# Kernel tuning notes

Hardware: AMD Instinct MI355X
Metric: run time of the kernel (lower is better)

Reference implementation:

```python
import jax, jax.numpy as jnp
import numpy as np


def recursive_fht(x):
    # Faithful vectorized version of the module's recursive butterfly FHT
    # (twiddle = cas(2*pi*n/N), no flipped-odd term, exactly as in the source).
    N = x.shape[-1]
    if N == 1:
        return x
    e = recursive_fht(x[..., ::2])
    o = recursive_fht(x[..., 1::2])
    n = jnp.arange(N // 2, dtype=x.dtype)
    t = jnp.cos(2 * jnp.pi * n / N) + jnp.sin(2 * jnp.pi * n / N)
    return jnp.concatenate([e + t * o, e - t * o], axis=-1)


def compl_mul1d(x1, x2):
    # x1: [B, i, modes], x2: [i, o, modes]; flips along axis 0 as in the source
    x1f = x1[::-1]
    x2f = x2[::-1]
    return 0.5 * (jnp.einsum('bix,iox->box', x1, x2)
                  - jnp.einsum('bix,iox->box', x1f, x2f)
                  + jnp.einsum('bix,iox->box', x1, x2f)
                  + jnp.einsum('bix,iox->box', x1f, x2))


def idht(X):
    # Inverse discrete Hartley transform via the cas matrix (DHT is an
    # involution up to 1/K). K = N//2+1 is not a power of 2, so a dense
    # transform is used. Compute-bound batched GEMM.
    K = X.shape[-1]
    n = jnp.arange(K, dtype=X.dtype)
    ang = 2.0 * jnp.pi * jnp.outer(n, n) / K
    cas = jnp.cos(ang) + jnp.sin(ang)  # [K, K]
    return jnp.einsum('bck,kn->bcn', X, cas) / K


def setup_inputs() -> dict:
    key = jax.random.key(0)
    k1, k2 = jax.random.split(key)
    B, Cin, Cout, N, modes1 = 32, 64, 64, 4096, 1024
    x = jax.random.normal(k1, (B, Cin, N), dtype=jnp.float32)
    scale = 1.0 / (Cin * Cout)
    weights1 = scale * jax.random.uniform(k2, (Cin, Cout, modes1), dtype=jnp.float32)
    return {"x": x, "weights1": weights1, "modes1": modes1}


def reference(x, weights1, modes1):
    B, C, N = x.shape
    # dht with threshold=1.0: FHT along last axis, low-pass filter is a no-op
    x_ht = recursive_fht(x)
    K = N // 2 + 1
    out_ht = jnp.zeros((B, C, K), dtype=x.dtype)
    out_ht = out_ht.at[:, :, :modes1].set(compl_mul1d(x_ht[:, :, :modes1], weights1))
    return idht(out_ht)  # [B, C, N//2+1]
```

## Files before the change

kernel.cpp:

```cpp
#include <hip/hip_runtime.h>
#include <hip/hip_bf16.h>

#define BATCH 32
#define CIN   64
#define COUT  64
#define NFFT  4096
#define MODES 1024
#define KOUT  2049
#define NPAD  2112

typedef __bf16 bf16x8 __attribute__((ext_vector_type(8)));
typedef float  f32x4  __attribute__((ext_vector_type(4)));

#define AS1 __attribute__((address_space(1)))
#define AS3 __attribute__((address_space(3)))

static __device__ __forceinline__ void gl_lds16(const void* g, void* l) {
    __builtin_amdgcn_global_load_lds((const AS1 void*)g, (AS3 void*)l, 16, 0, 0);
}

static __device__ __forceinline__ float bf2f(unsigned short s) {
    return __uint_as_float(((unsigned)s) << 16);
}
static __device__ __forceinline__ void cvt8(bf16x8 v, f32x4& lo, f32x4& hi) {
    union { bf16x8 b; unsigned short s[8]; } u;
    u.b = v;
    lo = (f32x4){bf2f(u.s[0]), bf2f(u.s[1]), bf2f(u.s[2]), bf2f(u.s[3])};
    hi = (f32x4){bf2f(u.s[4]), bf2f(u.s[5]), bf2f(u.s[6]), bf2f(u.s[7])};
}
static __device__ __forceinline__ bf16x8 pack8(f32x4 lo, f32x4 hi) {
    union { bf16x8 b; unsigned short s[8]; } u;
    __hip_bfloat16 h;
    h = __float2bfloat16(lo.x); u.s[0] = *(unsigned short*)&h;
    h = __float2bfloat16(lo.y); u.s[1] = *(unsigned short*)&h;
    h = __float2bfloat16(lo.z); u.s[2] = *(unsigned short*)&h;
    h = __float2bfloat16(lo.w); u.s[3] = *(unsigned short*)&h;
    h = __float2bfloat16(hi.x); u.s[4] = *(unsigned short*)&h;
    h = __float2bfloat16(hi.y); u.s[5] = *(unsigned short*)&h;
    h = __float2bfloat16(hi.z); u.s[6] = *(unsigned short*)&h;
    h = __float2bfloat16(hi.w); u.s[7] = *(unsigned short*)&h;
    return u.b;
}

static __device__ __forceinline__ void bfly4(float eA, float eB, float oA, float oB,
                                             float t, float c0, float c1,
                                             float& w0, float& w1, float& w2, float& w3) {
    float PA = fmaf(t, oA, eA), MA = fmaf(-t, oA, eA);
    float PB = fmaf(t, oB, eB), MB = fmaf(-t, oB, eB);
    w0 = fmaf(c0, PB, PA);
    w2 = fmaf(-c0, PB, PA);
    w1 = fmaf(c1, MB, MA);
    w3 = fmaf(-c1, MB, MA);
}

#define NCHUNK ((NPAD / 16) * (MODES / 32) * 64)

__global__ void fill_tables(float* __restrict__ tw, __hip_bfloat16* __restrict__ c2f) {
    int gid = blockIdx.x * 256 + threadIdx.x;
    if (gid < NCHUNK) {
        int nl  = gid & 15;
        int kc  = (gid >> 4) & 3;
        int blk = gid >> 6;
        int kb  = blk & 31;
        int gn  = blk >> 5;
        int n = gn * 16 + nl;
        int kbase = kb * 32 + kc * 8;
        unsigned short v8[8];
        if (n < KOUT) {
#pragma unroll
            for (int j = 0; j < 8; ++j) {
                int k = kbase + j;
                int m = (k * n) % KOUT;
                float ang = 6.28318530717958647692f * (float)m / (float)KOUT;
                float v = (cosf(ang) + sinf(ang)) * (1.0f / (float)KOUT);
                __hip_bfloat16 h = __float2bfloat16(v);
                v8[j] = *(unsigned short*)&h;
            }
        } else {
#pragma unroll
            for (int j = 0; j < 8; ++j) v8[j] = 0;
        }
        *(ushort4*)((char*)c2f + (size_t)gid * 16)     = make_ushort4(v8[0], v8[1], v8[2], v8[3]);
        *(ushort4*)((char*)c2f + (size_t)gid * 16 + 8) = make_ushort4(v8[4], v8[5], v8[6], v8[7]);
    } else {
        int t = gid - NCHUNK;
        if (t < NFFT) {
            if (t == 0) { tw[0] = 1.0f; return; }
            int h = 1 << (31 - __clz(t));
            int n = t - h;
            float ang = 3.14159265358979323846f * (float)n / (float)h;
            tw[t] = cosf(ang) + sinf(ang);
        }
    }
}

__global__ __launch_bounds__(256) void fht_kernel(const float* __restrict__ x,
                                                  const float* __restrict__ tw,
                                                  __hip_bfloat16* __restrict__ xh) {
    __shared__ float ldsA[4352];
    __shared__ float ldsB[4352];
    const int t = threadIdx.x;
    const int row = blockIdx.x;
    const float* xr = x + (size_t)row * NFFT;

    float r[4][4];
#pragma unroll
    for (int a = 0; a < 4; ++a)
#pragma unroll
        for (int c = 0; c < 4; ++c)
            r[a][c] = xr[t + 256 * a + 1024 * c];

    float o1[4][4];
#pragma unroll
    for (int a = 0; a < 4; ++a) {
        float PA = r[a][0] + r[a][2], MA = r[a][0] - r[a][2];
        float PB = r[a][1] + r[a][3], MB = r[a][1] - r[a][3];
        o1[a][0] = PA + PB;
        o1[a][2] = PA - PB;
        o1[a][1] = MA + MB;
        o1[a][3] = MA - MB;
    }
    float o2[4][4];
#pragma unroll
    for (int kap = 0; kap < 4; ++kap) {
        float tt = tw[4 + kap], c0 = tw[8 + kap], c1 = tw[12 + kap];
        bfly4(o1[0][kap], o1[1][kap], o1[2][kap], o1[3][kap], tt, c0, c1,
              o2[kap][0], o2[kap][1], o2[kap][2], o2[kap][3]);
    }
#pragma unroll
    for (int kap = 0; kap < 4; ++kap)
#pragma unroll
        for (int c = 0; c < 4; ++c) {
            int p = t + 256 * kap + 1024 * c;
            ldsA[p + (p >> 4)] = o2[kap][c];
        }
    __syncthreads();

    const int kap2 = t >> 4, gp = t & 15;
    float r2[4][4];
#pragma unroll
    for (int a = 0; a < 4; ++a)
#pragma unroll
        for (int c = 0; c < 4; ++c) {
            int p = 256 * kap2 + gp + 16 * a + 64 * c;
            r2[a][c] = ldsA[p + (p >> 4)];
        }
    float o3[4][4];
    {
        float tt = tw[16 + kap2], c0 = tw[32 + kap2], c1 = tw[48 + kap2];
#pragma unroll
        for (int a = 0; a < 4; ++a)
            bfly4(r2[a][0], r2[a][1], r2[a][2], r2[a][3], tt, c0, c1,
                  o3[a][0], o3[a][1], o3[a][2], o3[a][3]);
    }
    float o4[4][4];
#pragma unroll
    for (int c = 0; c < 4; ++c) {
        int kap3 = kap2 + 16 * c;
        float tt = tw[64 + kap3], c0 = tw[128 + kap3], c1 = tw[192 + kap3];
        bfly4(o3[0][c], o3[1][c], o3[2][c], o3[3][c], tt, c0, c1,
              o4[c][0], o4[c][1], o4[c][2], o4[c][3]);
    }
#pragma unroll
    for (int c = 0; c < 4; ++c)
#pragma unroll
        for (int cc = 0; cc < 4; ++cc) {
            int p = t + 256 * c + 1024 * cc;
            ldsB[p + (p >> 4)] = o4[c][cc];
        }
    __syncthreads();

    float r3[4][4];
#pragma unroll
    for (int g = 0; g < 4; ++g)
#pragma unroll
        for (int c = 0; c < 4; ++c) {
            int p = 16 * t + g + 4 * c;
            r3[g][c] = ldsB[p + (p >> 4)];
        }
    float o5[4][4];
    {
        float tt = tw[256 + t], c0 = tw[512 + t], c1 = tw[768 + t];
#pragma unroll
        for (int g = 0; g < 4; ++g)
            bfly4(r3[g][0], r3[g][1], r3[g][2], r3[g][3], tt, c0, c1,
                  o5[g][0], o5[g][1], o5[g][2], o5[g][3]);
    }
    __hip_bfloat16* xo = xh + (size_t)row * MODES;
#pragma unroll
    for (int c = 0; c < 4; ++c) {
        float tt = tw[1024 + t + 256 * c];
        float c0 = tw[2048 + t + 256 * c];
        float PA = fmaf(tt, o5[2][c], o5[0][c]);
        float PB = fmaf(tt, o5[3][c], o5[1][c]);
        xo[t + 256 * c] = __float2bfloat16(fmaf(c0, PB, PA));
    }
}

__global__ __launch_bounds__(512) void mix_kernel(const __hip_bfloat16* __restrict__ xh,
                                                  const float* __restrict__ w,
                                                  __hip_bfloat16* __restrict__ y) {
    const int tid = threadIdx.x;
    const int kl  = tid & 1;
    const int og  = (tid >> 1) & 31;
    const int bpl = tid >> 6;
    const int bp  = blockIdx.y * 8 + bpl;
    const int rb  = (BATCH - 1) - bp;
    const int o   = blockIdx.z * 32 + og;
    const int k8  = blockIdx.x * 2 + kl;

    f32x4 accb0 = {0,0,0,0}, accb1 = {0,0,0,0};
    f32x4 accr0 = {0,0,0,0}, accr1 = {0,0,0,0};

    const __hip_bfloat16* xb  = xh + (size_t)(bp * CIN) * MODES + k8 * 8;
    const __hip_bfloat16* xrb = xh + (size_t)(rb * CIN) * MODES + k8 * 8;
    const float* wo = w + (size_t)o * MODES + k8 * 8;

#pragma unroll 4
    for (int i = 0; i < 32; ++i) {
        const int mi = 63 - i;
        bf16x8 xai = *(const bf16x8*)(xb  + (size_t)i  * MODES);
        bf16x8 xam = *(const bf16x8*)(xb  + (size_t)mi * MODES);
        bf16x8 xbi = *(const bf16x8*)(xrb + (size_t)i  * MODES);
        bf16x8 xbm = *(const bf16x8*)(xrb + (size_t)mi * MODES);
        f32x4 w1a = *(const f32x4*)(wo + (size_t)(i  * COUT) * MODES);
        f32x4 w1b = *(const f32x4*)(wo + (size_t)(i  * COUT) * MODES + 4);
        f32x4 w2a = *(const f32x4*)(wo + (size_t)(mi * COUT) * MODES);
        f32x4 w2b = *(const f32x4*)(wo + (size_t)(mi * COUT) * MODES + 4);

        f32x4 ai_lo, ai_hi, am_lo, am_hi, bi_lo, bi_hi, bm_lo, bm_hi;
        cvt8(xai, ai_lo, ai_hi);
        cvt8(xam, am_lo, am_hi);
        cvt8(xbi, bi_lo, bi_hi);
        cvt8(xbm, bm_lo, bm_hi);

        f32x4 sa0 = ai_lo + am_lo, sa1 = ai_hi + am_hi;
        f32x4 da0 = ai_lo - am_lo, da1 = ai_hi - am_hi;
        f32x4 sb0 = bi_lo + bm_lo, sb1 = bi_hi + bm_hi;
        f32x4 db0 = bi_lo - bm_lo, db1 = bi_hi - bm_hi;
        f32x4 wp0 = w1a + w2a, wm0 = w1a - w2a;
        f32x4 wp1 = w1b + w2b, wm1 = w1b - w2b;

        accb0 += sa0 * wp0 + db0 * wm0;
        accb1 += sa1 * wp1 + db1 * wm1;
        accr0 += sb0 * wp0 + da0 * wm0;
        accr1 += sb1 * wp1 + da1 * wm1;
    }

    bf16x8 vb = pack8(accb0 * 0.5f, accb1 * 0.5f);
    bf16x8 vr = pack8(accr0 * 0.5f, accr1 * 0.5f);
    *(bf16x8*)(y + (size_t)(bp * COUT + o) * MODES + k8 * 8) = vb;
    *(bf16x8*)(y + (size_t)(rb * COUT + o) * MODES + k8 * 8) = vr;
}

__global__ __launch_bounds__(128) void idht_mfma(const __hip_bfloat16* __restrict__ yh,
                                                 const __hip_bfloat16* __restrict__ c2f,
                                                 float* __restrict__ out) {
    __shared__ __align__(16) char sa[2][4 * 1024];

    const int tid  = threadIdx.x;
    const int lane = tid & 63;
    const int wave = tid >> 6;
    const int rbase = blockIdx.x * 64;
    const int gn0   = blockIdx.y * 4;
    const int nbase = gn0 * 16;

    const int lrow = (lane & 15) * 2048;
    const int lchk = (lane >> 4) * 16;

    const char* ga = (const char*)yh + (size_t)rbase * 2048;
    const char* gb = (const char*)c2f;

    f32x4 acc[2][4];
#pragma unroll
    for (int mt = 0; mt < 2; ++mt)
#pragma unroll
        for (int nt = 0; nt < 4; ++nt) acc[mt][nt] = (f32x4){0.f, 0.f, 0.f, 0.f};

    auto stageA = [&](int bi, int k0) {
#pragma unroll
        for (int r = 0; r < 2; ++r) {
            int g = wave * 2 + r;
            gl_lds16(ga + (size_t)(g * 16) * 2048 + lrow + lchk + k0 * 2,
                     sa[bi] + g * 1024);
        }
    };
    auto loadB = [&](int ks, bf16x8* b_) {
#pragma unroll
        for (int nt = 0; nt < 4; ++nt) {
            size_t ch = ((size_t)(gn0 + nt) * 32 + ks) * 64 + lane;
            b_[nt] = *(const bf16x8*)(gb + ch * 16);
        }
    };

    stageA(0, 0);
    bf16x8 bcur[4];
    loadB(0, bcur);
    int cur = 0;
    for (int ks = 0; ks < MODES / 32; ++ks) {
        __syncthreads();
        if (ks + 1 < MODES / 32) stageA(cur ^ 1, (ks + 1) * 32);
        bf16x8 bnext[4];
        int kn = (ks + 1 < MODES / 32) ? ks + 1 : ks;
        loadB(kn, bnext);
        bf16x8 a_[2];
#pragma unroll
        for (int mt = 0; mt < 2; ++mt)
            a_[mt] = *(const bf16x8*)(sa[cur] + (wave * 2 + mt) * 1024 + lane * 16);
#pragma unroll
        for (int mt = 0; mt < 2; ++mt)
#pragma unroll
            for (int nt = 0; nt < 4; ++nt)
                acc[mt][nt] = __builtin_amdgcn_mfma_f32_16x16x32_bf16(a_[mt], bcur[nt], acc[mt][nt], 0, 0, 0);
#pragma unroll
        for (int nt = 0; nt < 4; ++nt) bcur[nt] = bnext[nt];
        cur ^= 1;
    }

#pragma unroll
    for (int mt = 0; mt < 2; ++mt) {
        int row = rbase + wave * 32 + mt * 16 + (lane >> 4) * 4;
#pragma unroll
        for (int nt = 0; nt < 4; ++nt) {
            int col = nbase + nt * 16 + (lane & 15);
            if (col < KOUT) {
#pragma unroll
                for (int r = 0; r < 4; ++r)
                    out[(size_t)(row + r) * KOUT + col] = acc[mt][nt][r];
            }
        }
    }
}

extern "C" void kernel_launch(void* const* d_in, const int* in_sizes, int n_in,
                              void* d_out, int out_size, void* d_ws, size_t ws_size,
                              hipStream_t stream) {
    const float* x = (const float*)d_in[0];
    const float* w = (const float*)d_in[1];
    float* out = (float*)d_out;

    float* tw = (float*)d_ws;
    __hip_bfloat16* xh  = (__hip_bfloat16*)(tw + NFFT);
    __hip_bfloat16* y   = xh + (size_t)BATCH * CIN * MODES;
    __hip_bfloat16* c2f = y + (size_t)BATCH * COUT * MODES;

    fill_tables<<<(NCHUNK + NFFT + 255) / 256, 256, 0, stream>>>(tw, c2f);
    fht_kernel<<<BATCH * CIN, 256, 0, stream>>>(x, tw, xh);
    mix_kernel<<<dim3(64, 2, 2), 512, 0, stream>>>(xh, w, y);
    idht_mfma<<<dim3((BATCH * COUT) / 64, NPAD / 64), 128, 0, stream>>>(y, c2f, out);
}
```

Measured before the change: 160.4 us.

## Replace LDS staging in IDHT GEMM with register prefetch; remap mix grid

The IDHT MFMA kernel drops its LDS double buffer and per-iteration barrier. Each lane now loads its A and B fragments straight from global memory into a three-deep register ring, prefetching three k-steps ahead inside a fully unrolled loop. The mixing kernel is remapped so each block handles one batch pair, 4 output channels and 64 k-chunks, launched on many more blocks of 256 threads. The intent is to remove synchronisation and LDS round-trip latency and to raise occupancy, at the cost of more VGPRs, a larger unrolled body, and uncoalesced 16-byte A reads that are no longer shared through LDS.

```diff
diff --git a/kernel.cpp b/kernel.cpp
--- a/kernel.cpp
+++ b/kernel.cpp
@@ -11,13 +11,6 @@
 
 typedef __bf16 bf16x8 __attribute__((ext_vector_type(8)));
 typedef float  f32x4  __attribute__((ext_vector_type(4)));
-
-#define AS1 __attribute__((address_space(1)))
-#define AS3 __attribute__((address_space(3)))
-
-static __device__ __forceinline__ void gl_lds16(const void* g, void* l) {
-    __builtin_amdgcn_global_load_lds((const AS1 void*)g, (AS3 void*)l, 16, 0, 0);
-}
 
 static __device__ __forceinline__ float bf2f(unsigned short s) {
     return __uint_as_float(((unsigned)s) << 16);
@@ -197,17 +190,15 @@
     }
 }
 
-__global__ __launch_bounds__(512) void mix_kernel(const __hip_bfloat16* __restrict__ xh,
+__global__ __launch_bounds__(256) void mix_kernel(const __hip_bfloat16* __restrict__ xh,
                                                   const float* __restrict__ w,
                                                   __hip_bfloat16* __restrict__ y) {
-    const int tid = threadIdx.x;
-    const int kl  = tid & 1;
-    const int og  = (tid >> 1) & 31;
-    const int bpl = tid >> 6;
-    const int bp  = blockIdx.y * 8 + bpl;
-    const int rb  = (BATCH - 1) - bp;
-    const int o   = blockIdx.z * 32 + og;
-    const int k8  = blockIdx.x * 2 + kl;
+    const int kl = threadIdx.x & 63;
+    const int jg = threadIdx.x >> 6;
+    const int k8 = blockIdx.x * 64 + kl;
+    const int bp = blockIdx.y;
+    const int rb = (BATCH - 1) - bp;
+    const int o  = blockIdx.z * 4 + jg;
 
     f32x4 accb0 = {0,0,0,0}, accb1 = {0,0,0,0};
     f32x4 accr0 = {0,0,0,0}, accr1 = {0,0,0,0};
@@ -256,8 +247,6 @@
 __global__ __launch_bounds__(128) void idht_mfma(const __hip_bfloat16* __restrict__ yh,
                                                  const __hip_bfloat16* __restrict__ c2f,
                                                  float* __restrict__ out) {
-    __shared__ __align__(16) char sa[2][4 * 1024];
-
     const int tid  = threadIdx.x;
     const int lane = tid & 63;
     const int wave = tid >> 6;
@@ -265,11 +254,9 @@
     const int gn0   = blockIdx.y * 4;
     const int nbase = gn0 * 16;
 
-    const int lrow = (lane & 15) * 2048;
-    const int lchk = (lane >> 4) * 16;
-
-    const char* ga = (const char*)yh + (size_t)rbase * 2048;
-    const char* gb = (const char*)c2f;
+    const char* ga = (const char*)yh + (size_t)rbase * 2048
+                   + (size_t)(wave * 32 + (lane & 15)) * 2048 + (lane >> 4) * 16;
+    const char* gb = (const char*)c2f + ((size_t)gn0 * 32 * 64 + lane) * 16;
 
     f32x4 acc[2][4];
 #pragma unroll
@@ -277,53 +264,41 @@
 #pragma unroll
         for (int nt = 0; nt < 4; ++nt) acc[mt][nt] = (f32x4){0.f, 0.f, 0.f, 0.f};
 
-    auto stageA = [&](int bi, int k0) {
-#pragma unroll
-        for (int r = 0; r < 2; ++r) {
-            int g = wave * 2 + r;
-            gl_lds16(ga + (size_t)(g * 16) * 2048 + lrow + lchk + k0 * 2,
-                     sa[bi] + g * 1024);
-        }
-    };
-    auto loadB = [&](int ks, bf16x8* b_) {
-#pragma unroll
-        for (int nt = 0; nt < 4; ++nt) {
-            size_t ch = ((size_t)(gn0 + nt) * 32 + ks) * 64 + lane;
-            b_[nt] = *(const bf16x8*)(gb + ch * 16);
-        }
-    };
-
-    stageA(0, 0);
-    bf16x8 bcur[4];
-    loadB(0, bcur);
-    int cur = 0;
+    bf16x8 af[3][2], bf[3][4];
+
+#define LOADS(ks, s)                                                              \
+    {                                                                             \
+        _Pragma("unroll")                                                         \
+        for (int mt = 0; mt < 2; ++mt)                                            \
+            af[s][mt] = *(const bf16x8*)(ga + (size_t)mt * 16 * 2048 + (ks) * 64);\
+        _Pragma("unroll")                                                         \
+        for (int nt = 0; nt < 4; ++nt)                                            \
+            bf[s][nt] = *(const bf16x8*)(gb + ((size_t)nt * 32 + (ks)) * 1024);   \
+    }
+
+    LOADS(0, 0)
+    LOADS(1, 1)
+    LOADS(2, 2)
+#pragma unroll
     for (int ks = 0; ks < MODES / 32; ++ks) {
-        __syncthreads();
-        if (ks + 1 < MODES / 32) stageA(cur ^ 1, (ks + 1) * 32);
-        bf16x8 bnext[4];
-        int kn = (ks + 1 < MODES / 32) ? ks + 1 : ks;
-        loadB(kn, bnext);
-        bf16x8 a_[2];
+        const int s = ks % 3;
 #pragma unroll
         for (int mt = 0; mt < 2; ++mt)
-            a_[mt] = *(const bf16x8*)(sa[cur] + (wave * 2 + mt) * 1024 + lane * 16);
-#pragma unroll
-        for (int mt = 0; mt < 2; ++mt)
 #pragma unroll
             for (int nt = 0; nt < 4; ++nt)
-                acc[mt][nt] = __builtin_amdgcn_mfma_f32_16x16x32_bf16(a_[mt], bcur[nt], acc[mt][nt], 0, 0, 0);
-#pragma unroll
-        for (int nt = 0; nt < 4; ++nt) bcur[nt] = bnext[nt];
-        cur ^= 1;
-    }
-
+                acc[mt][nt] = __builtin_amdgcn_mfma_f32_16x16x32_bf16(af[s][mt], bf[s][nt], acc[mt][nt], 0, 0, 0);
+        if (ks + 3 < MODES / 32) LOADS(ks + 3, s)
+    }
+#undef LOADS
+
+    const bool full = (nbase + 64 <= KOUT);
 #pragma unroll
     for (int mt = 0; mt < 2; ++mt) {
         int row = rbase + wave * 32 + mt * 16 + (lane >> 4) * 4;
 #pragma unroll
         for (int nt = 0; nt < 4; ++nt) {
             int col = nbase + nt * 16 + (lane & 15);
-            if (col < KOUT) {
+            if (full || col < KOUT) {
 #pragma unroll
                 for (int r = 0; r < 4; ++r)
                     out[(size_t)(row + r) * KOUT + col] = acc[mt][nt][r];
@@ -346,6 +321,6 @@
 
     fill_tables<<<(NCHUNK + NFFT + 255) / 256, 256, 0, stream>>>(tw, c2f);
     fht_kernel<<<BATCH * CIN, 256, 0, stream>>>(x, tw, xh);
-    mix_kernel<<<dim3(64, 2, 2), 512, 0, stream>>>(xh, w, y);
+    mix_kernel<<<dim3(2, 16, 16), 256, 0, stream>>>(xh, w, y);
     idht_mfma<<<dim3((BATCH * COUT) / 64, NPAD / 64), 128, 0, stream>>>(y, c2f, out);
 }
```

After: 146.0 us. 9.0% less time.
